# Optimization experiments

Measured on AMD Instinct MI355X. Metric: run time of the kernel, lower is better.

## Reference

```python
import jax, jax.numpy as jnp
import numpy as np

H = 1024
F = 4096  # base_ffn_dim = hidden * 4
WIDTHS = [256, 512]  # adapters; idx 2 -> width==hidden -> identity
EPS = 1e-5


def _xavier(key, fan_in, fan_out, gain):
    a = gain * np.sqrt(6.0 / (fan_in + fan_out))
    return jax.random.uniform(key, (fan_in, fan_out), jnp.float32, -a, a)


def _layernorm(x, g, b):
    mu = jnp.mean(x, axis=-1, keepdims=True)
    var = jnp.var(x, axis=-1, keepdims=True)
    return (x - mu) * jax.lax.rsqrt(var + EPS) * g + b


def setup_inputs() -> dict:
    key = jax.random.key(0)
    ks = jax.random.split(key, 12)
    g = 1.0 / np.sqrt(2.0)
    B, S = 4, 2048
    return {
        "x": jax.random.normal(ks[0], (B, S, H), jnp.float32),
        "width_multiplier": jax.random.uniform(ks[1], (B, S, 1), jnp.float32),
        "width_idx": jax.random.randint(ks[2], (B, S), 0, 3, jnp.int32),
        "ln_in_g": jnp.ones((H,), jnp.float32),
        "ln_in_b": jnp.zeros((H,), jnp.float32),
        "W1": _xavier(ks[3], H, F, g),
        "b1": jnp.zeros((F,), jnp.float32),
        "ln_h_g": jnp.ones((F,), jnp.float32),
        "ln_h_b": jnp.zeros((F,), jnp.float32),
        "W2": _xavier(ks[4], F, H, g),
        "b2": jnp.zeros((H,), jnp.float32),
        "a256_w1": _xavier(ks[5], H, 256, g),
        "a256_b1": jnp.zeros((256,), jnp.float32),
        "a256_w2": _xavier(ks[6], 256, H, g),
        "a256_b2": jnp.zeros((H,), jnp.float32),
        "a512_w1": _xavier(ks[7], H, 512, g),
        "a512_b1": jnp.zeros((512,), jnp.float32),
        "a512_w2": _xavier(ks[8], 512, H, g),
        "a512_b2": jnp.zeros((H,), jnp.float32),
    }


def reference(x, width_multiplier, width_idx,
              ln_in_g, ln_in_b, W1, b1, ln_h_g, ln_h_b, W2, b2,
              a256_w1, a256_b1, a256_w2, a256_b2,
              a512_w1, a512_b1, a512_w2, a512_b2):
    gelu = lambda t: jax.nn.gelu(t, approximate=False)  # torch nn.GELU exact
    x_norm = _layernorm(x, ln_in_g, ln_in_b)
    # base FFN path
    h = gelu(jnp.einsum("bsh,hf->bsf", x_norm, W1) + b1)
    h = _layernorm(h, ln_h_g, ln_h_b)
    base = jnp.einsum("bsf,fh->bsh", h, W2) + b2
    # width adapters (routed per token by width_idx)
    ad0 = jnp.einsum("bsw,wh->bsh", gelu(jnp.einsum("bsh,hw->bsw", x_norm, a256_w1) + a256_b1), a256_w2) + a256_b2
    ad1 = jnp.einsum("bsw,wh->bsh", gelu(jnp.einsum("bsh,hw->bsw", x_norm, a512_w1) + a512_b1), a512_w2) + a512_b2
    idx = width_idx[..., None]
    adaptive = jnp.where(idx == 0, ad0, jnp.where(idx == 1, ad1, x_norm))
    return base * width_multiplier + adaptive * (1.0 - width_multiplier)
```

## Files before the change

### kernel.cpp

```cpp
#include <hip/hip_runtime.h>
#include <cstdint>
#include <cstddef>

typedef unsigned short u16x8 __attribute__((ext_vector_type(8)));
typedef __bf16 bf16x8 __attribute__((ext_vector_type(8)));
typedef float f32x4 __attribute__((ext_vector_type(4)));

__device__ __forceinline__ float b2f(unsigned short u) {
    union { unsigned int i; float f; } v;
    v.i = ((unsigned int)u) << 16;
    return v.f;
}

__device__ __forceinline__ unsigned short f2b(float f) {
    union { float f; unsigned int i; } v;
    v.f = f;
    unsigned int x = v.i;
    unsigned int lsb = (x >> 16) & 1u;
    x += 0x7FFFu + lsb;
    return (unsigned short)(x >> 16);
}

__device__ __forceinline__ float gelu_exact(float x) {
    return 0.5f * x * (1.0f + erff(x * 0.70710678118654752f));
}

__device__ __forceinline__ void ld_lds16(const unsigned short* g, unsigned short* l) {
    __builtin_amdgcn_global_load_lds(
        (const __attribute__((address_space(1))) void*)g,
        (__attribute__((address_space(3))) void*)l, 16, 0, 0);
}

__global__ void transpose_f32_bf16(const float* __restrict__ in,
                                   unsigned short* __restrict__ out, int R, int C) {
    __shared__ float tile[32][33];
    int x = blockIdx.x * 32 + threadIdx.x;
    int y0 = blockIdx.y * 32;
    for (int k = 0; k < 32; k += 8)
        tile[threadIdx.y + k][threadIdx.x] = in[(size_t)(y0 + threadIdx.y + k) * C + x];
    __syncthreads();
    int ox = y0 + threadIdx.x;
    int oy = blockIdx.x * 32;
    for (int k = 0; k < 32; k += 8)
        out[(size_t)(oy + threadIdx.y + k) * R + ox] = f2b(tile[threadIdx.x][threadIdx.y + k]);
}

__global__ void concat_bias(const float* __restrict__ b0, const float* __restrict__ b1,
                            float* __restrict__ out) {
    int t = threadIdx.x + blockIdx.x * blockDim.x;
    if (t < 256) out[t] = b0[t];
    else if (t < 768) out[t] = b1[t - 256];
}

__device__ __forceinline__ float ldf(const float* p, int i) { return p[i]; }
__device__ __forceinline__ float ldf(const unsigned short* p, int i) { return b2f(p[i]); }

template <int NPT, typename TIN>
__global__ __launch_bounds__(256) void ln_rows(const TIN* __restrict__ in,
                                               unsigned short* __restrict__ out,
                                               const float* __restrict__ g,
                                               const float* __restrict__ b) {
    const int ncol = NPT * 256;
    const int row = blockIdx.x;
    const int t = threadIdx.x;
    const TIN* xr = in + (size_t)row * ncol;

    float v[NPT];
    float s = 0.f, s2 = 0.f;
#pragma unroll
    for (int i = 0; i < NPT; ++i) {
        float f = ldf(xr, t + (i << 8));
        v[i] = f;
        s += f;
        s2 += f * f;
    }
#pragma unroll
    for (int o = 32; o > 0; o >>= 1) {
        s  += __shfl_down(s, o, 64);
        s2 += __shfl_down(s2, o, 64);
    }
    __shared__ float red[8];
    int lane = t & 63, w = t >> 6;
    if (lane == 0) { red[w] = s; red[4 + w] = s2; }
    __syncthreads();
    if (t == 0) {
        red[0] = red[0] + red[1] + red[2] + red[3];
        red[4] = red[4] + red[5] + red[6] + red[7];
    }
    __syncthreads();
    float inv_n = 1.0f / (float)ncol;
    float mu = red[0] * inv_n;
    float var = red[4] * inv_n - mu * mu;
    float rs = rsqrtf(var + 1e-5f);

    unsigned short* orow = out + (size_t)row * ncol;
#pragma unroll
    for (int i = 0; i < NPT; ++i) {
        int c = t + (i << 8);
        orow[c] = f2b((v[i] - mu) * rs * g[c] + b[c]);
    }
}

template <int EPI>
__global__ __launch_bounds__(256) void gemm_bt(
    const unsigned short* __restrict__ A, int lda,
    const unsigned short* __restrict__ BT, int ldb,
    const float* __restrict__ bias, unsigned short* __restrict__ Cb,
    float* __restrict__ Cf, int M, int N, int K,
    const int* __restrict__ idx, int match,
    const float* __restrict__ wm,
    const unsigned short* __restrict__ adaptive,
    const unsigned short* __restrict__ xn) {
    __shared__ __align__(16) unsigned short As[2][128 * 32];
    __shared__ __align__(16) unsigned short Bs[2][128 * 32];

    const int t = threadIdx.x;
    const int m0 = blockIdx.y * 128;
    const int n0 = blockIdx.x * 128;

    const int lane = t & 63;
    const int wid = t >> 6;

    const int srow = lane >> 2;
    const int sch  = (lane & 3) ^ (srow & 3);
    const int scol = sch << 3;

    const int wr = (wid >> 1) << 6;
    const int wc = (wid & 1) << 6;
    const int ml = lane & 15;
    const int q = lane >> 4;
    const int qsw = ((q ^ (ml & 3)) << 3);

    f32x4 acc[4][4];
#pragma unroll
    for (int i = 0; i < 4; ++i)
#pragma unroll
        for (int j = 0; j < 4; ++j)
#pragma unroll
            for (int r = 0; r < 4; ++r) acc[i][j][r] = 0.0f;

    const int nk = K >> 5;

#define STAGE(KT, BUF)                                                          \
    {                                                                           \
        _Pragma("unroll")                                                       \
        for (int hh = 0; hh < 2; ++hh) {                                        \
            int rbase = wid * 32 + hh * 16;                                     \
            int row = rbase + srow;                                             \
            ld_lds16(A  + (size_t)(m0 + row) * lda + (KT) * 32 + scol,          \
                     &As[BUF][rbase * 32]);                                     \
            ld_lds16(BT + (size_t)(n0 + row) * ldb + (KT) * 32 + scol,          \
                     &Bs[BUF][rbase * 32]);                                     \
        }                                                                       \
    }

    STAGE(0, 0);
    for (int kt = 0; kt < nk; ++kt) {
        const int cur = kt & 1;
        __syncthreads();
        if (kt + 1 < nk) STAGE(kt + 1, cur ^ 1);

        bf16x8 af[4], bf[4];
#pragma unroll
        for (int i = 0; i < 4; ++i)
            af[i] = *(const bf16x8*)(&As[cur][(wr + i * 16 + ml) * 32 + qsw]);
#pragma unroll
        for (int j = 0; j < 4; ++j)
            bf[j] = *(const bf16x8*)(&Bs[cur][(wc + j * 16 + ml) * 32 + qsw]);
#pragma unroll
        for (int i = 0; i < 4; ++i)
#pragma unroll
            for (int j = 0; j < 4; ++j)
                acc[i][j] = __builtin_amdgcn_mfma_f32_16x16x32_bf16(af[i], bf[j], acc[i][j], 0, 0, 0);
    }
#undef STAGE

#pragma unroll
    for (int i = 0; i < 4; ++i) {
#pragma unroll
        for (int j = 0; j < 4; ++j) {
            int col = n0 + wc + j * 16 + ml;
            float bv = bias[col];
#pragma unroll
            for (int r = 0; r < 4; ++r) {
                int row = m0 + wr + i * 16 + q * 4 + r;
                float val = acc[i][j][r] + bv;
                size_t off = (size_t)row * N + col;
                if (EPI == 0) {
                    Cb[off] = f2b(gelu_exact(val));
                } else if (EPI == 1) {
                    if (idx[row] == match) Cb[off] = f2b(val);
                } else {
                    float w = wm[row];
                    int id = idx[row];
                    float a = b2f((id <= 1) ? adaptive[off] : xn[off]);
                    Cf[off] = val * w + a * (1.0f - w);
                }
            }
        }
    }
}

extern "C" void kernel_launch(void* const* d_in, const int* in_sizes, int n_in,
                              void* d_out, int out_size, void* d_ws, size_t ws_size,
                              hipStream_t stream) {
    const float* x       = (const float*)d_in[0];
    const float* wm      = (const float*)d_in[1];
    const int*   widx    = (const int*)d_in[2];
    const float* ln_in_g = (const float*)d_in[3];
    const float* ln_in_b = (const float*)d_in[4];
    const float* W1      = (const float*)d_in[5];
    const float* b1      = (const float*)d_in[6];
    const float* ln_h_g  = (const float*)d_in[7];
    const float* ln_h_b  = (const float*)d_in[8];
    const float* W2      = (const float*)d_in[9];
    const float* b2      = (const float*)d_in[10];
    const float* a256_w1 = (const float*)d_in[11];
    const float* a256_b1 = (const float*)d_in[12];
    const float* a256_w2 = (const float*)d_in[13];
    const float* a256_b2 = (const float*)d_in[14];
    const float* a512_w1 = (const float*)d_in[15];
    const float* a512_b1 = (const float*)d_in[16];
    const float* a512_w2 = (const float*)d_in[17];
    const float* a512_b2 = (const float*)d_in[18];
    float* out = (float*)d_out;

    const int T = 8192, H = 1024, F = 4096;

    unsigned short* ws0   = (unsigned short*)d_ws;
    unsigned short* xn    = ws0;
    unsigned short* h     = xn    + (size_t)T * H;
    unsigned short* tt    = h     + (size_t)T * F;
    unsigned short* adp   = tt    + (size_t)T * 768;
    unsigned short* W1T   = adp   + (size_t)T * H;
    unsigned short* W2T   = W1T   + (size_t)H * F;
    unsigned short* awup  = W2T   + (size_t)F * H;
    unsigned short* aw2T0 = awup  + (size_t)768 * H;
    unsigned short* aw2T1 = aw2T0 + (size_t)H * 256;
    float*          ab1   = (float*)(aw2T1 + (size_t)H * 512);

    dim3 tb(32, 8);
    transpose_f32_bf16<<<dim3(F / 32,   H / 32), tb, 0, stream>>>(W1, W1T, H, F);
    transpose_f32_bf16<<<dim3(H / 32,   F / 32), tb, 0, stream>>>(W2, W2T, F, H);
    transpose_f32_bf16<<<dim3(256 / 32, H / 32), tb, 0, stream>>>(a256_w1, awup, H, 256);
    transpose_f32_bf16<<<dim3(512 / 32, H / 32), tb, 0, stream>>>(a512_w1, awup + (size_t)256 * H, H, 512);
    transpose_f32_bf16<<<dim3(H / 32, 256 / 32), tb, 0, stream>>>(a256_w2, aw2T0, 256, H);
    transpose_f32_bf16<<<dim3(H / 32, 512 / 32), tb, 0, stream>>>(a512_w2, aw2T1, 512, H);
    concat_bias<<<3, 256, 0, stream>>>(a256_b1, a512_b1, ab1);

    ln_rows<4, float><<<T, 256, 0, stream>>>(x, xn, ln_in_g, ln_in_b);

    gemm_bt<0><<<dim3(F / 128, T / 128), 256, 0, stream>>>(
        xn, H, W1T, H, b1, h, nullptr, T, F, H, nullptr, 0, nullptr, nullptr, nullptr);

    gemm_bt<0><<<dim3(768 / 128, T / 128), 256, 0, stream>>>(
        xn, H, awup, H, ab1, tt, nullptr, T, 768, H, nullptr, 0, nullptr, nullptr, nullptr);

    gemm_bt<1><<<dim3(H / 128, T / 128), 256, 0, stream>>>(
        tt, 768, aw2T0, 256, a256_b2, adp, nullptr, T, H, 256, widx, 0, nullptr, nullptr, nullptr);
    gemm_bt<1><<<dim3(H / 128, T / 128), 256, 0, stream>>>(
        tt + 256, 768, aw2T1, 512, a512_b2, adp, nullptr, T, H, 512, widx, 1, nullptr, nullptr, nullptr);

    ln_rows<16, unsigned short><<<T, 256, 0, stream>>>(h, h, ln_h_g, ln_h_b);

    gemm_bt<2><<<dim3(H / 128, T / 128), 256, 0, stream>>>(
        h, F, W2T, F, b2, nullptr, out, T, H, F, widx, 0, wm, adp, xn);
}
```

Before: 453.3 us.

## Route adapter GEMMs by gathered row lists and fold hidden LayerNorm into W2 epilogue

Builds per-adapter token row lists with atomics so the adapter up and down GEMMs only process tokens routed to each adapter, scattering results back by row index. The hidden LayerNorm is algebraically folded: gamma is premultiplied into W2, per-row mean/rstd come from a read-only stats pass, and column sums of gamma*W2 and beta*W2 correct the GEMM output in the epilogue. This removes the in-place LN read/write of the large hidden tensor and roughly two-thirds of adapter FLOPs. It also vectorizes the input LayerNorm. The risk is added precision error from the mean subtraction being done after the bf16 GEMM, plus nondeterministic row ordering from atomics.

Measured after the change: 598.5 us. +32.0%, slower.

```diff
diff --git a/kernel.cpp b/kernel.cpp
--- a/kernel.cpp
+++ b/kernel.cpp
@@ -3,6 +3,7 @@
 #include <cstddef>
 
 typedef unsigned short u16x8 __attribute__((ext_vector_type(8)));
+typedef unsigned short u16x4 __attribute__((ext_vector_type(4)));
 typedef __bf16 bf16x8 __attribute__((ext_vector_type(8)));
 typedef float f32x4 __attribute__((ext_vector_type(4)));
 
@@ -32,12 +33,16 @@
 }
 
 __global__ void transpose_f32_bf16(const float* __restrict__ in,
-                                   unsigned short* __restrict__ out, int R, int C) {
+                                   unsigned short* __restrict__ out, int R, int C,
+                                   const float* __restrict__ scale) {
     __shared__ float tile[32][33];
     int x = blockIdx.x * 32 + threadIdx.x;
     int y0 = blockIdx.y * 32;
-    for (int k = 0; k < 32; k += 8)
-        tile[threadIdx.y + k][threadIdx.x] = in[(size_t)(y0 + threadIdx.y + k) * C + x];
+    for (int k = 0; k < 32; k += 8) {
+        float v = in[(size_t)(y0 + threadIdx.y + k) * C + x];
+        if (scale) v *= scale[y0 + threadIdx.y + k];
+        tile[threadIdx.y + k][threadIdx.x] = v;
+    }
     __syncthreads();
     int ox = y0 + threadIdx.x;
     int oy = blockIdx.x * 32;
@@ -45,35 +50,44 @@
         out[(size_t)(oy + threadIdx.y + k) * R + ox] = f2b(tile[threadIdx.x][threadIdx.y + k]);
 }
 
-__global__ void concat_bias(const float* __restrict__ b0, const float* __restrict__ b1,
-                            float* __restrict__ out) {
-    int t = threadIdx.x + blockIdx.x * blockDim.x;
-    if (t < 256) out[t] = b0[t];
-    else if (t < 768) out[t] = b1[t - 256];
-}
-
-__device__ __forceinline__ float ldf(const float* p, int i) { return p[i]; }
-__device__ __forceinline__ float ldf(const unsigned short* p, int i) { return b2f(p[i]); }
-
-template <int NPT, typename TIN>
-__global__ __launch_bounds__(256) void ln_rows(const TIN* __restrict__ in,
-                                               unsigned short* __restrict__ out,
-                                               const float* __restrict__ g,
-                                               const float* __restrict__ b) {
-    const int ncol = NPT * 256;
-    const int row = blockIdx.x;
-    const int t = threadIdx.x;
-    const TIN* xr = in + (size_t)row * ncol;
-
-    float v[NPT];
-    float s = 0.f, s2 = 0.f;
-#pragma unroll
-    for (int i = 0; i < NPT; ++i) {
-        float f = ldf(xr, t + (i << 8));
-        v[i] = f;
-        s += f;
-        s2 += f * f;
-    }
+__global__ void init_misc(float* __restrict__ S, float* __restrict__ cv,
+                          int* __restrict__ cnt) {
+    int t = blockIdx.x * 256 + threadIdx.x;
+    if (t < 1024) { S[t] = 0.f; cv[t] = 0.f; }
+    if (t < 2) cnt[t] = 0;
+}
+
+__global__ void colreduce_w2(const float* __restrict__ W2, const float* __restrict__ g,
+                             const float* __restrict__ b, float* __restrict__ S,
+                             float* __restrict__ cv) {
+    int c = blockIdx.x * 256 + threadIdx.x;
+    int f0 = blockIdx.y * 256;
+    float s = 0.f, cc = 0.f;
+    for (int f = f0; f < f0 + 256; ++f) {
+        float w = W2[(size_t)f * 1024 + c];
+        s = fmaf(g[f], w, s);
+        cc = fmaf(b[f], w, cc);
+    }
+    atomicAdd(&S[c], s);
+    atomicAdd(&cv[c], cc);
+}
+
+__global__ void build_lists(const int* __restrict__ widx, int* __restrict__ cnt,
+                            int* __restrict__ rl0, int* __restrict__ rl1) {
+    int i = blockIdx.x * 256 + threadIdx.x;
+    int id = widx[i];
+    if (id == 0)      rl0[atomicAdd(&cnt[0], 1)] = i;
+    else if (id == 1) rl1[atomicAdd(&cnt[1], 1)] = i;
+}
+
+__global__ __launch_bounds__(256) void ln1024(const float* __restrict__ x,
+                                              unsigned short* __restrict__ xn,
+                                              const float* __restrict__ g,
+                                              const float* __restrict__ b) {
+    const int row = blockIdx.x, t = threadIdx.x;
+    const float4 v = ((const float4*)(x + (size_t)row * 1024))[t];
+    float s = v.x + v.y + v.z + v.w;
+    float s2 = v.x * v.x + v.y * v.y + v.z * v.z + v.w * v.w;
 #pragma unroll
     for (int o = 32; o > 0; o >>= 1) {
         s  += __shfl_down(s, o, 64);
@@ -88,16 +102,47 @@
         red[4] = red[4] + red[5] + red[6] + red[7];
     }
     __syncthreads();
-    float inv_n = 1.0f / (float)ncol;
-    float mu = red[0] * inv_n;
-    float var = red[4] * inv_n - mu * mu;
+    float mu = red[0] * (1.0f / 1024.0f);
+    float var = red[4] * (1.0f / 1024.0f) - mu * mu;
     float rs = rsqrtf(var + 1e-5f);
-
-    unsigned short* orow = out + (size_t)row * ncol;
-#pragma unroll
-    for (int i = 0; i < NPT; ++i) {
-        int c = t + (i << 8);
-        orow[c] = f2b((v[i] - mu) * rs * g[c] + b[c]);
+    float4 gg = ((const float4*)g)[t];
+    float4 bb = ((const float4*)b)[t];
+    u16x4 o;
+    o[0] = f2b((v.x - mu) * rs * gg.x + bb.x);
+    o[1] = f2b((v.y - mu) * rs * gg.y + bb.y);
+    o[2] = f2b((v.z - mu) * rs * gg.z + bb.z);
+    o[3] = f2b((v.w - mu) * rs * gg.w + bb.w);
+    ((u16x4*)(xn + (size_t)row * 1024))[t] = o;
+}
+
+__global__ __launch_bounds__(256) void row_stats(const unsigned short* __restrict__ h,
+                                                 float* __restrict__ mu,
+                                                 float* __restrict__ rs) {
+    const int row = blockIdx.x, t = threadIdx.x;
+    const u16x8* hv = (const u16x8*)(h + (size_t)row * 4096);
+    float s = 0.f, s2 = 0.f;
+#pragma unroll
+    for (int i = 0; i < 2; ++i) {
+        u16x8 v = hv[t + i * 256];
+#pragma unroll
+        for (int e = 0; e < 8; ++e) { float f = b2f(v[e]); s += f; s2 += f * f; }
+    }
+#pragma unroll
+    for (int o = 32; o > 0; o >>= 1) {
+        s  += __shfl_down(s, o, 64);
+        s2 += __shfl_down(s2, o, 64);
+    }
+    __shared__ float red[8];
+    int lane = t & 63, w = t >> 6;
+    if (lane == 0) { red[w] = s; red[4 + w] = s2; }
+    __syncthreads();
+    if (t == 0) {
+        float S  = red[0] + red[1] + red[2] + red[3];
+        float S2 = red[4] + red[5] + red[6] + red[7];
+        float m = S * (1.0f / 4096.0f);
+        float var = S2 * (1.0f / 4096.0f) - m * m;
+        mu[row] = m;
+        rs[row] = rsqrtf(var + 1e-5f);
     }
 }
 
@@ -105,19 +150,26 @@
 __global__ __launch_bounds__(256) void gemm_bt(
     const unsigned short* __restrict__ A, int lda,
     const unsigned short* __restrict__ BT, int ldb,
-    const float* __restrict__ bias, unsigned short* __restrict__ Cb,
-    float* __restrict__ Cf, int M, int N, int K,
-    const int* __restrict__ idx, int match,
-    const float* __restrict__ wm,
-    const unsigned short* __restrict__ adaptive,
-    const unsigned short* __restrict__ xn) {
+    const float* __restrict__ bias,
+    unsigned short* __restrict__ Cb, float* __restrict__ Cf, int N, int K,
+    const int* __restrict__ rlist, const int* __restrict__ cnt,
+    const int* __restrict__ idx, const float* __restrict__ wm,
+    const unsigned short* __restrict__ adp, const unsigned short* __restrict__ xn,
+    const float* __restrict__ mu, const float* __restrict__ rs,
+    const float* __restrict__ Svec, const float* __restrict__ cvec) {
     __shared__ __align__(16) unsigned short As[2][128 * 32];
     __shared__ __align__(16) unsigned short Bs[2][128 * 32];
 
-    const int t = threadIdx.x;
     const int m0 = blockIdx.y * 128;
     const int n0 = blockIdx.x * 128;
 
+    int cnt_ = 0;
+    if (EPI == 1 || EPI == 2) {
+        cnt_ = *cnt;
+        if (m0 >= cnt_) return;
+    }
+
+    const int t = threadIdx.x;
     const int lane = t & 63;
     const int wid = t >> 6;
 
@@ -131,6 +183,18 @@
     const int q = lane >> 4;
     const int qsw = ((q ^ (ml & 3)) << 3);
 
+    const unsigned short* aptr[2];
+    const unsigned short* bptr[2];
+#pragma unroll
+    for (int hh = 0; hh < 2; ++hh) {
+        int grow = m0 + wid * 32 + hh * 16 + srow;
+        int arow;
+        if (EPI == 1) arow = (grow < cnt_) ? rlist[grow] : 0;
+        else          arow = grow;
+        aptr[hh] = A  + (size_t)arow * lda + scol;
+        bptr[hh] = BT + (size_t)(n0 + wid * 32 + hh * 16 + srow) * ldb + scol;
+    }
+
     f32x4 acc[4][4];
 #pragma unroll
     for (int i = 0; i < 4; ++i)
@@ -146,11 +210,8 @@
         _Pragma("unroll")                                                       \
         for (int hh = 0; hh < 2; ++hh) {                                        \
             int rbase = wid * 32 + hh * 16;                                     \
-            int row = rbase + srow;                                             \
-            ld_lds16(A  + (size_t)(m0 + row) * lda + (KT) * 32 + scol,          \
-                     &As[BUF][rbase * 32]);                                     \
-            ld_lds16(BT + (size_t)(n0 + row) * ldb + (KT) * 32 + scol,          \
-                     &Bs[BUF][rbase * 32]);                                     \
+            ld_lds16(aptr[hh] + (KT) * 32, &As[BUF][rbase * 32]);               \
+            ld_lds16(bptr[hh] + (KT) * 32, &Bs[BUF][rbase * 32]);               \
         }                                                                       \
     }
 
@@ -181,20 +242,24 @@
         for (int j = 0; j < 4; ++j) {
             int col = n0 + wc + j * 16 + ml;
             float bv = bias[col];
+            float sv = 0.f, cvv = 0.f;
+            if (EPI == 3) { sv = Svec[col]; cvv = cvec[col]; }
 #pragma unroll
             for (int r = 0; r < 4; ++r) {
                 int row = m0 + wr + i * 16 + q * 4 + r;
-                float val = acc[i][j][r] + bv;
                 size_t off = (size_t)row * N + col;
-                if (EPI == 0) {
-                    Cb[off] = f2b(gelu_exact(val));
-                } else if (EPI == 1) {
-                    if (idx[row] == match) Cb[off] = f2b(val);
+                if (EPI == 0 || EPI == 1) {
+                    Cb[off] = f2b(gelu_exact(acc[i][j][r] + bv));
+                } else if (EPI == 2) {
+                    if (row < cnt_)
+                        Cb[(size_t)rlist[row] * N + col] = f2b(acc[i][j][r] + bv);
                 } else {
+                    float rr = rs[row];
+                    float v2 = rr * acc[i][j][r] - rr * mu[row] * sv + cvv + bv;
                     float w = wm[row];
                     int id = idx[row];
-                    float a = b2f((id <= 1) ? adaptive[off] : xn[off]);
-                    Cf[off] = val * w + a * (1.0f - w);
+                    float a = b2f((id <= 1) ? adp[off] : xn[off]);
+                    Cf[off] = v2 * w + a * (1.0f - w);
                 }
             }
         }
@@ -230,39 +295,59 @@
     unsigned short* ws0   = (unsigned short*)d_ws;
     unsigned short* xn    = ws0;
     unsigned short* h     = xn    + (size_t)T * H;
-    unsigned short* tt    = h     + (size_t)T * F;
-    unsigned short* adp   = tt    + (size_t)T * 768;
+    unsigned short* tc0   = h     + (size_t)T * F;
+    unsigned short* tc1   = tc0   + (size_t)(T + 128) * 256;
+    unsigned short* adp   = tc1   + (size_t)(T + 128) * 512;
     unsigned short* W1T   = adp   + (size_t)T * H;
     unsigned short* W2T   = W1T   + (size_t)H * F;
-    unsigned short* awup  = W2T   + (size_t)F * H;
-    unsigned short* aw2T0 = awup  + (size_t)768 * H;
+    unsigned short* aw1T0 = W2T   + (size_t)F * H;
+    unsigned short* aw1T1 = aw1T0 + (size_t)256 * H;
+    unsigned short* aw2T0 = aw1T1 + (size_t)512 * H;
     unsigned short* aw2T1 = aw2T0 + (size_t)H * 256;
-    float*          ab1   = (float*)(aw2T1 + (size_t)H * 512);
+    float* fbase = (float*)(aw2T1 + (size_t)H * 512);
+    float* Svec  = fbase;
+    float* cvec  = Svec + 1024;
+    float* muv   = cvec + 1024;
+    float* rsv   = muv + 8192;
+    int*   cnts  = (int*)(rsv + 8192);
+    int*   rl0   = cnts + 2;
+    int*   rl1   = rl0 + 8192;
 
     dim3 tb(32, 8);
-    transpose_f32_bf16<<<dim3(F / 32,   H / 32), tb, 0, stream>>>(W1, W1T, H, F);
-    transpose_f32_bf16<<<dim3(H / 32,   F / 32), tb, 0, stream>>>(W2, W2T, F, H);
-    transpose_f32_bf16<<<dim3(256 / 32, H / 32), tb, 0, stream>>>(a256_w1, awup, H, 256);
-    transpose_f32_bf16<<<dim3(512 / 32, H / 32), tb, 0, stream>>>(a512_w1, awup + (size_t)256 * H, H, 512);
-    transpose_f32_bf16<<<dim3(H / 32, 256 / 32), tb, 0, stream>>>(a256_w2, aw2T0, 256, H);
-    transpose_f32_bf16<<<dim3(H / 32, 512 / 32), tb, 0, stream>>>(a512_w2, aw2T1, 512, H);
-    concat_bias<<<3, 256, 0, stream>>>(a256_b1, a512_b1, ab1);
-
-    ln_rows<4, float><<<T, 256, 0, stream>>>(x, xn, ln_in_g, ln_in_b);
+    transpose_f32_bf16<<<dim3(F / 32,   H / 32), tb, 0, stream>>>(W1, W1T, H, F, nullptr);
+    transpose_f32_bf16<<<dim3(H / 32,   F / 32), tb, 0, stream>>>(W2, W2T, F, H, ln_h_g);
+    transpose_f32_bf16<<<dim3(256 / 32, H / 32), tb, 0, stream>>>(a256_w1, aw1T0, H, 256, nullptr);
+    transpose_f32_bf16<<<dim3(512 / 32, H / 32), tb, 0, stream>>>(a512_w1, aw1T1, H, 512, nullptr);
+    transpose_f32_bf16<<<dim3(H / 32, 256 / 32), tb, 0, stream>>>(a256_w2, aw2T0, 256, H, nullptr);
+    transpose_f32_bf16<<<dim3(H / 32, 512 / 32), tb, 0, stream>>>(a512_w2, aw2T1, 512, H, nullptr);
+
+    init_misc<<<4, 256, 0, stream>>>(Svec, cvec, cnts);
+    colreduce_w2<<<dim3(4, 16), 256, 0, stream>>>(W2, ln_h_g, ln_h_b, Svec, cvec);
+    build_lists<<<32, 256, 0, stream>>>(widx, cnts, rl0, rl1);
+
+    ln1024<<<T, 256, 0, stream>>>(x, xn, ln_in_g, ln_in_b);
+
+    gemm_bt<1><<<dim3(2, 64), 256, 0, stream>>>(
+        xn, H, aw1T0, H, a256_b1, tc0, nullptr, 256, H,
+        rl0, cnts + 0, nullptr, nullptr, nullptr, nullptr, nullptr, nullptr, nullptr, nullptr);
+    gemm_bt<1><<<dim3(4, 64), 256, 0, stream>>>(
+        xn, H, aw1T1, H, a512_b1, tc1, nullptr, 512, H,
+        rl1, cnts + 1, nullptr, nullptr, nullptr, nullptr, nullptr, nullptr, nullptr, nullptr);
+
+    gemm_bt<2><<<dim3(8, 64), 256, 0, stream>>>(
+        tc0, 256, aw2T0, 256, a256_b2, adp, nullptr, H, 256,
+        rl0, cnts + 0, nullptr, nullptr, nullptr, nullptr, nullptr, nullptr, nullptr, nullptr);
+    gemm_bt<2><<<dim3(8, 64), 256, 0, stream>>>(
+        tc1, 512, aw2T1, 512, a512_b2, adp, nullptr, H, 512,
+        rl1, cnts + 1, nullptr, nullptr, nullptr, nullptr, nullptr, nullptr, nullptr, nullptr);
 
     gemm_bt<0><<<dim3(F / 128, T / 128), 256, 0, stream>>>(
-        xn, H, W1T, H, b1, h, nullptr, T, F, H, nullptr, 0, nullptr, nullptr, nullptr);
-
-    gemm_bt<0><<<dim3(768 / 128, T / 128), 256, 0, stream>>>(
-        xn, H, awup, H, ab1, tt, nullptr, T, 768, H, nullptr, 0, nullptr, nullptr, nullptr);
-
-    gemm_bt<1><<<dim3(H / 128, T / 128), 256, 0, stream>>>(
-        tt, 768, aw2T0, 256, a256_b2, adp, nullptr, T, H, 256, widx, 0, nullptr, nullptr, nullptr);
-    gemm_bt<1><<<dim3(H / 128, T / 128), 256, 0, stream>>>(
-        tt + 256, 768, aw2T1, 512, a512_b2, adp, nullptr, T, H, 512, widx, 1, nullptr, nullptr, nullptr);
-
-    ln_rows<16, unsigned short><<<T, 256, 0, stream>>>(h, h, ln_h_g, ln_h_b);
-
-    gemm_bt<2><<<dim3(H / 128, T / 128), 256, 0, stream>>>(
-        h, F, W2T, F, b2, nullptr, out, T, H, F, widx, 0, wm, adp, xn);
-}
+        xn, H, W1T, H, b1, h, nullptr, F, H,
+        nullptr, nullptr, nullptr, nullptr, nullptr, nullptr, nullptr, nullptr, nullptr, nullptr);
+
+    row_stats<<<T, 256, 0, stream>>>(h, muv, rsv);
+
+    gemm_bt<3><<<dim3(H / 128, T / 128), 256, 0, stream>>>(
+        h, F, W2T, F, b2, nullptr, out, H, F,
+        nullptr, nullptr, widx, wm, adp, xn, muv, rsv, Svec, cvec);
+}
```
